# Kernel tuning notes

Hardware: AMD Instinct MI355X
Metric: run time of the kernel (lower is better)

Reference implementation:

```python
import jax, jax.numpy as jnp
import numpy as np

EMBED_DIM = 768
NUM_HEADS = 12
HEAD_DIM = EMBED_DIM // NUM_HEADS
SCALER = HEAD_DIM ** (-0.5)


def setup_inputs() -> dict:
    key = jax.random.key(0)
    k_x, k_wqkv, k_wo = jax.random.split(key, 3)
    B, N, C = 8, 1024, EMBED_DIM
    # GlorotUniform limits
    lim_qkv = (6.0 / (C + 3 * C)) ** 0.5
    lim_o = (6.0 / (C + C)) ** 0.5
    return {
        "inputs": jax.random.normal(k_x, (B, N, C), dtype=jnp.float32),
        "w_qkv": jax.random.uniform(k_wqkv, (C, 3 * C), minval=-lim_qkv, maxval=lim_qkv, dtype=jnp.float32),
        "b_qkv": jnp.zeros((3 * C,), dtype=jnp.float32),
        "w_out": jax.random.uniform(k_wo, (C, C), minval=-lim_o, maxval=lim_o, dtype=jnp.float32),
        "b_out": jnp.zeros((C,), dtype=jnp.float32),
    }


def reference(inputs, w_qkv, b_qkv, w_out, b_out):
    B, N, C = inputs.shape
    H, D = NUM_HEADS, C // NUM_HEADS
    qkv = inputs @ w_qkv + b_qkv                      # [B, N, 3C]
    qkv = qkv.reshape(B, N, 3, H, D).transpose(2, 0, 3, 1, 4)  # [3, B, H, N, D]
    q, k, v = qkv[0], qkv[1], qkv[2]
    scores = jnp.einsum("bhnd,bhmd->bhnm", q, k) * SCALER      # [B, H, N, N]
    attn = jax.nn.softmax(scores, axis=-1)
    x = jnp.einsum("bhnm,bhmd->bhnd", attn, v)                  # [B, H, N, D]
    x = x.transpose(0, 2, 1, 3).reshape(B, N, C)
    return x @ w_out + b_out
```

## Files before the change

kernel.cpp:

```cpp
#include <hip/hip_runtime.h>
#include <hip/hip_bf16.h>
#include <cstdint>
#include <cstddef>

#define EMBED 768
#define NHEADS 12
#define HDIM 64
#define SEQ 1024
#define BATCH 8

typedef __attribute__((ext_vector_type(8))) short bf16x8;
typedef __attribute__((ext_vector_type(4))) float f32x4;
typedef __attribute__((ext_vector_type(16))) float f32x16;
typedef __attribute__((ext_vector_type(4))) unsigned int u32x4;

__device__ __forceinline__ short f2bf(float f) {
    union { float f; uint32_t u; } x; x.f = f;
    uint32_t r = x.u + 0x7fffu + ((x.u >> 16) & 1u);
    return (short)(r >> 16);
}

__device__ __forceinline__ unsigned int cvt_pk_bf16(float lo, float hi) {
    unsigned int r;
    asm("v_cvt_pk_bf16_f32 %0, %1, %2" : "=v"(r) : "v"(lo), "v"(hi));
    return r;
}

__device__ __forceinline__ void permswap(unsigned int& a, unsigned int& b) {
    asm volatile("v_permlane32_swap_b32 %0, %1" : "+v"(a), "+v"(b));
}

__device__ __forceinline__ void gload_lds16(const void* g, void* l) {
    __builtin_amdgcn_global_load_lds(
        (const __attribute__((address_space(1))) unsigned int*)g,
        (__attribute__((address_space(3))) unsigned int*)l, 16, 0, 0);
}

__global__ __launch_bounds__(256) void convert_bf16(
    const float* __restrict__ in, short* __restrict__ out) {
    size_t i = ((size_t)blockIdx.x * 256 + threadIdx.x) * 8;
    float4 a = *reinterpret_cast<const float4*>(in + i);
    float4 b = *reinterpret_cast<const float4*>(in + i + 4);
    bf16x8 v;
    v[0] = f2bf(a.x); v[1] = f2bf(a.y); v[2] = f2bf(a.z); v[3] = f2bf(a.w);
    v[4] = f2bf(b.x); v[5] = f2bf(b.y); v[6] = f2bf(b.z); v[7] = f2bf(b.w);
    *reinterpret_cast<bf16x8*>(out + i) = v;
}

__global__ __launch_bounds__(256) void transpose_conv(
    const float* __restrict__ in, short* __restrict__ out, int R, int C) {
    __shared__ float tile[64][65];
    const int tid = threadIdx.x;
    const int c0 = blockIdx.x * 64, r0 = blockIdx.y * 64;
#pragma unroll
    for (int i = 0; i < 16; ++i) {
        int e = tid + 256 * i;
        int r = e >> 6, c = e & 63;
        tile[r][c] = in[(size_t)(r0 + r) * C + c0 + c];
    }
    __syncthreads();
#pragma unroll
    for (int i = 0; i < 16; ++i) {
        int e = tid + 256 * i;
        int rr = e >> 6, cc = e & 63;
        out[(size_t)(c0 + rr) * R + r0 + cc] = f2bf(tile[cc][rr]);
    }
}

__global__ __launch_bounds__(256) void gemm_qkv(
    const short* __restrict__ A, const short* __restrict__ Bt,
    const float* __restrict__ bias,
    short* __restrict__ Qo, short* __restrict__ Ko, short* __restrict__ Vto) {
    __shared__ __align__(16) char smem[65536];
    const int tid = threadIdx.x;
    const int lane = tid & 63;
    const int wid = tid >> 6;
    const int wm = wid >> 1, wn = wid & 1;
    const int bid = blockIdx.x;
    const int wg = (bid & 7) * 144 + (bid >> 3);
    const int mb = wg / 18, nb = wg - mb * 18;
    const int m0 = mb * 128;
    const int n0 = nb * 128;

    const f32x4 zero4 = {0.f, 0.f, 0.f, 0.f};
    f32x4 acc[4][4];
#pragma unroll
    for (int i = 0; i < 4; ++i)
#pragma unroll
        for (int j = 0; j < 4; ++j) acc[i][j] = zero4;

    const short* Ab = A + (size_t)m0 * EMBED;
    const short* Bb = Bt + (size_t)n0 * EMBED;

    auto stage = [&](int p, int kt) {
        const int k0 = kt * 64;
        char* base = smem + p * 32768;
#pragma unroll
        for (int i = 0; i < 4; ++i) {
            int e = i * 256 + tid;
            int r = e >> 3, cs = (e & 7) ^ (r & 7);
            char* dst = base + (size_t)(i * 256 + wid * 64) * 16;
            gload_lds16(Ab + (size_t)r * EMBED + k0 + cs * 8, dst);
            gload_lds16(Bb + (size_t)r * EMBED + k0 + cs * 8, dst + 16384);
        }
    };

    stage(0, 0);
    stage(1, 1);
    asm volatile("s_waitcnt vmcnt(8)" ::: "memory");
    __builtin_amdgcn_s_barrier();
    __builtin_amdgcn_sched_barrier(0);

    for (int t = 0; t < 12; ++t) {
        const int p = t & 1;
        const char* As = smem + p * 32768;
        const char* Bs = As + 16384;
        bf16x8 af[4][2], bfv[4][2];
#pragma unroll
        for (int mi = 0; mi < 4; ++mi)
#pragma unroll
            for (int kh = 0; kh < 2; ++kh) {
                int row = wm * 64 + mi * 16 + (lane & 15);
                int c = kh * 4 + (lane >> 4);
                af[mi][kh] = *reinterpret_cast<const bf16x8*>(
                    As + row * 128 + (((c ^ (row & 7))) << 4));
            }
#pragma unroll
        for (int ni = 0; ni < 4; ++ni)
#pragma unroll
            for (int kh = 0; kh < 2; ++kh) {
                int row = wn * 64 + ni * 16 + (lane & 15);
                int c = kh * 4 + (lane >> 4);
                bfv[ni][kh] = *reinterpret_cast<const bf16x8*>(
                    Bs + row * 128 + (((c ^ (row & 7))) << 4));
            }
        asm volatile("s_waitcnt lgkmcnt(0)" ::: "memory");
        __builtin_amdgcn_s_barrier();
        __builtin_amdgcn_sched_barrier(0);
        if (t + 2 < 12) stage(p, t + 2);

        __builtin_amdgcn_s_setprio(1);
#pragma unroll
        for (int mi = 0; mi < 4; ++mi)
#pragma unroll
            for (int ni = 0; ni < 4; ++ni)
#pragma unroll
                for (int kh = 0; kh < 2; ++kh)
                    acc[mi][ni] = __builtin_amdgcn_mfma_f32_16x16x32_bf16(
                        af[mi][kh], bfv[ni][kh], acc[mi][ni], 0, 0, 0);
        __builtin_amdgcn_s_setprio(0);

        if (t + 2 < 12)
            asm volatile("s_waitcnt vmcnt(8)" ::: "memory");
        else
            asm volatile("s_waitcnt vmcnt(0)" ::: "memory");
        __builtin_amdgcn_s_barrier();
        __builtin_amdgcn_sched_barrier(0);
    }

    const int s = nb / 6;
    const int bb = m0 >> 10;
    if (s == 2) {
        char* T = smem;
#pragma unroll
        for (int mi = 0; mi < 4; ++mi)
#pragma unroll
            for (int ni = 0; ni < 4; ++ni)
#pragma unroll
                for (int rp = 0; rp < 2; ++rp) {
                    int ml = wm * 64 + mi * 16 + ((lane >> 4) << 2) + rp * 2;
                    int nl = wn * 64 + ni * 16 + (lane & 15);
                    float bsv = bias[n0 + nl];
                    unsigned int w = cvt_pk_bf16(acc[mi][ni][rp * 2] + bsv,
                                                 acc[mi][ni][rp * 2 + 1] + bsv);
                    *reinterpret_cast<unsigned int*>(
                        T + nl * 256 + ((ml * 2) ^ ((nl & 7) << 4))) = w;
                }
        __syncthreads();
        short* Vrow0 = Vto + ((size_t)bb * 768 + (nb - 12) * 128) * SEQ + (m0 & 1023);
#pragma unroll
        for (int it = 0; it < 8; ++it) {
            int chunk = it * 256 + tid;
            int row = chunk >> 4, k = chunk & 15;
            u32x4 v = *reinterpret_cast<const u32x4*>(
                T + row * 256 + ((k * 16) ^ ((row & 7) << 4)));
            *reinterpret_cast<u32x4*>(Vrow0 + (size_t)row * SEQ + k * 8) = v;
        }
    } else {
        short* dst = (s == 0) ? Qo : Ko;
        const float qs = (s == 0) ? 0.18033688f : 1.0f;
        const int rem0 = n0 - s * 768;
#pragma unroll
        for (int mi = 0; mi < 4; ++mi)
#pragma unroll
            for (int ni = 0; ni < 4; ++ni)
#pragma unroll
                for (int r = 0; r < 4; ++r) {
                    int m = m0 + wm * 64 + mi * 16 + ((lane >> 4) << 2) + r;
                    int nl = wn * 64 + ni * 16 + (lane & 15);
                    int rem = rem0 + nl;
                    int h = rem >> 6, d = rem & 63;
                    int tok = m & 1023;
                    float v = (acc[mi][ni][r] + bias[n0 + nl]) * qs;
                    dst[(((size_t)(bb * NHEADS + h)) * SEQ + tok) * HDIM + d] = f2bf(v);
                }
    }
}

__global__ __launch_bounds__(256) void attn_kernel(
    const short* __restrict__ Q, const short* __restrict__ K,
    const short* __restrict__ Vt, short* __restrict__ Xo) {
    __shared__ __align__(16) char smem[49152];
    const int tid = threadIdx.x, lane = tid & 63, wid = tid >> 6;
    const int l31 = lane & 31, g = lane >> 5;
    const int bh = blockIdx.x, qt = blockIdx.y;
    const int b = bh / NHEADS, h = bh - b * NHEADS;
    const short* Qh = Q + (size_t)bh * SEQ * HDIM;
    const short* Kh = K + (size_t)bh * SEQ * HDIM;
    const short* Vh = Vt + (size_t)bh * HDIM * SEQ;
    const int q0 = qt * 128 + wid * 32;
    const int swz = (l31 & 7);

    const f32x16 zero16 = 0.f;
    bf16x8 qf[4];
#pragma unroll
    for (int ds = 0; ds < 4; ++ds)
        qf[ds] = *reinterpret_cast<const bf16x8*>(
            Qh + (size_t)(q0 + l31) * HDIM + ds * 16 + g * 8);

    u32x4 onesw;
    onesw[0] = 0x3f803f80u; onesw[1] = 0x3f803f80u;
    onesw[2] = 0x3f803f80u; onesw[3] = 0x3f803f80u;
    const bf16x8 ones = __builtin_bit_cast(bf16x8, onesw);

    f32x16 o0 = zero16, o1 = zero16;
    f32x16 ls = zero16;

    auto stage = [&](int buf, int j0) {
#pragma unroll
        for (int i = 0; i < 2; ++i) {
            int e = i * 256 + tid;
            int r = e >> 3, cs = (e & 7) ^ (r & 7);
            char* dst = smem + (size_t)(i * 256 + wid * 64) * 16 + buf * 8192;
            gload_lds16(Kh + (size_t)(j0 + r) * HDIM + cs * 8, dst);
            gload_lds16(Vh + (size_t)r * SEQ + j0 + cs * 8, dst + 24576);
        }
    };

    stage(0, 0);
    stage(1, 64);

    for (int t = 0; t < 16; ++t) {
        const int bsel = t % 3;
        if (t < 15)
            asm volatile("s_waitcnt vmcnt(4)" ::: "memory");
        else
            asm volatile("s_waitcnt vmcnt(0)" ::: "memory");
        __builtin_amdgcn_s_barrier();
        __builtin_amdgcn_sched_barrier(0);

        const char* kb = smem + bsel * 8192;
        const char* vb = smem + 24576 + bsel * 8192;

        bf16x8 kf[2][4];
#pragma unroll
        for (int s = 0; s < 2; ++s)
#pragma unroll
            for (int ds = 0; ds < 4; ++ds)
                kf[s][ds] = *reinterpret_cast<const bf16x8*>(
                    kb + (s * 32 + l31) * 128 + (((ds * 2 + g) ^ swz) << 4));
        bf16x8 vf[4][2];
#pragma unroll
        for (int kst = 0; kst < 4; ++kst)
#pragma unroll
            for (int dsub = 0; dsub < 2; ++dsub)
                vf[kst][dsub] = *reinterpret_cast<const bf16x8*>(
                    vb + (dsub * 32 + l31) * 128 + (((kst * 2 + g) ^ swz) << 4));
        __builtin_amdgcn_sched_barrier(0);
        if (t + 2 < 16) stage((t + 2) % 3, (t + 2) * 64);

        f32x16 s0 = zero16, s1 = zero16;
        __builtin_amdgcn_s_setprio(1);
#pragma unroll
        for (int ds = 0; ds < 4; ++ds) {
            s0 = __builtin_amdgcn_mfma_f32_32x32x16_bf16(kf[0][ds], qf[ds], s0, 0, 0, 0);
            s1 = __builtin_amdgcn_mfma_f32_32x32x16_bf16(kf[1][ds], qf[ds], s1, 0, 0, 0);
        }
        __builtin_amdgcn_s_setprio(0);

#pragma unroll
        for (int r = 0; r < 16; ++r) {
            s0[r] = __builtin_amdgcn_exp2f(s0[r]);
            s1[r] = __builtin_amdgcn_exp2f(s1[r]);
        }

        bf16x8 pf[4];
#pragma unroll
        for (int s = 0; s < 2; ++s) {
            const f32x16& sv = s ? s1 : s0;
            unsigned int pk[8];
#pragma unroll
            for (int j = 0; j < 8; ++j) pk[j] = cvt_pk_bf16(sv[2 * j], sv[2 * j + 1]);
            permswap(pk[0], pk[2]); permswap(pk[1], pk[3]);
            permswap(pk[4], pk[6]); permswap(pk[5], pk[7]);
            u32x4 wlo, whi;
            wlo[0] = pk[0]; wlo[1] = pk[1]; wlo[2] = pk[2]; wlo[3] = pk[3];
            whi[0] = pk[4]; whi[1] = pk[5]; whi[2] = pk[6]; whi[3] = pk[7];
            pf[s * 2 + 0] = __builtin_bit_cast(bf16x8, wlo);
            pf[s * 2 + 1] = __builtin_bit_cast(bf16x8, whi);
        }

        __builtin_amdgcn_s_setprio(1);
#pragma unroll
        for (int kst = 0; kst < 4; ++kst) {
            o0 = __builtin_amdgcn_mfma_f32_32x32x16_bf16(vf[kst][0], pf[kst], o0, 0, 0, 0);
            o1 = __builtin_amdgcn_mfma_f32_32x32x16_bf16(vf[kst][1], pf[kst], o1, 0, 0, 0);
            ls = __builtin_amdgcn_mfma_f32_32x32x16_bf16(ones, pf[kst], ls, 0, 0, 0);
        }
        __builtin_amdgcn_s_setprio(0);
    }

    const float rl = 1.0f / ls[0];

    __syncthreads();
    char* T = smem;
    {
        char* Tw = T + (wid * 32 + l31) * 128;
        const int qx = (l31 & 7) << 4;
#pragma unroll
        for (int half = 0; half < 2; ++half) {
            const f32x16& ov = half ? o1 : o0;
#pragma unroll
            for (int j = 0; j < 8; ++j) {
                unsigned int w = cvt_pk_bf16(ov[2 * j] * rl, ov[2 * j + 1] * rl);
                int off = 4 * (j & 1) + 16 * (j >> 1) + 8 * g + 64 * half;
                *reinterpret_cast<unsigned int*>(Tw + (off ^ qx)) = w;
            }
        }
    }
    __syncthreads();
    const int q0b = qt * 128;
    short* xbase = Xo + ((size_t)b * SEQ + q0b) * EMBED + h * HDIM;
#pragma unroll
    for (int it = 0; it < 4; ++it) {
        int chunk = it * 256 + tid;
        int row = chunk >> 3, k = chunk & 7;
        u32x4 v = *reinterpret_cast<const u32x4*>(
            T + row * 128 + ((k * 16) ^ ((row & 7) << 4)));
        *reinterpret_cast<u32x4*>(xbase + (size_t)row * EMBED + k * 8) = v;
    }
}

__global__ __launch_bounds__(256) void gemm_out(
    const short* __restrict__ A, const short* __restrict__ Bt,
    const float* __restrict__ bias, float* __restrict__ C) {
    __shared__ __align__(16) char smem[49152];
    const int tid = threadIdx.x;
    const int lane = tid & 63;
    const int wid = tid >> 6;
    const int wm = wid >> 1, wn = wid & 1;
    const int bid = blockIdx.x;
    const int wg = (bid & 7) * 96 + (bid >> 3);
    const int mb = wg / 12, nb = wg - mb * 12;
    const int m0 = mb * 128;
    const int n0 = nb * 64;

    const f32x4 zero4 = {0.f, 0.f, 0.f, 0.f};
    f32x4 acc[4][2];
#pragma unroll
    for (int i = 0; i < 4; ++i)
#pragma unroll
        for (int j = 0; j < 2; ++j) acc[i][j] = zero4;

    const short* Ab = A + (size_t)m0 * EMBED;
    const short* Bb = Bt + (size_t)n0 * EMBED;

    auto stage = [&](int p, int kt) {
        const int k0 = kt * 64;
        char* base = smem + p * 24576;
#pragma unroll
        for (int i = 0; i < 4; ++i) {
            int e = i * 256 + tid;
            int r = e >> 3, cs = (e & 7) ^ (r & 7);
            gload_lds16(Ab + (size_t)r * EMBED + k0 + cs * 8,
                        base + (size_t)(i * 256 + wid * 64) * 16);
        }
#pragma unroll
        for (int i = 0; i < 2; ++i) {
            int e = i * 256 + tid;
            int r = e >> 3, cs = (e & 7) ^ (r & 7);
            gload_lds16(Bb + (size_t)r * EMBED + k0 + cs * 8,
                        base + 16384 + (size_t)(i * 256 + wid * 64) * 16);
        }
    };

    stage(0, 0);
    stage(1, 1);
    asm volatile("s_waitcnt vmcnt(6)" ::: "memory");
    __builtin_amdgcn_s_barrier();
    __builtin_amdgcn_sched_barrier(0);

    for (int t = 0; t < 12; ++t) {
        const int p = t & 1;
        const char* As = smem + p * 24576;
        const char* Bs = As + 16384;
        bf16x8 af[4][2], bfv[2][2];
#pragma unroll
        for (int mi = 0; mi < 4; ++mi)
#pragma unroll
            for (int kh = 0; kh < 2; ++kh) {
                int row = wm * 64 + mi * 16 + (lane & 15);
                int c = kh * 4 + (lane >> 4);
                af[mi][kh] = *reinterpret_cast<const bf16x8*>(
                    As + row * 128 + (((c ^ (row & 7))) << 4));
            }
#pragma unroll
        for (int ni = 0; ni < 2; ++ni)
#pragma unroll
            for (int kh = 0; kh < 2; ++kh) {
                int row = wn * 32 + ni * 16 + (lane & 15);
                int c = kh * 4 + (lane >> 4);
                bfv[ni][kh] = *reinterpret_cast<const bf16x8*>(
                    Bs + row * 128 + (((c ^ (row & 7))) << 4));
            }
        asm volatile("s_waitcnt lgkmcnt(0)" ::: "memory");
        __builtin_amdgcn_s_barrier();
        __builtin_amdgcn_sched_barrier(0);
        if (t + 2 < 12) stage(p, t + 2);

        __builtin_amdgcn_s_setprio(1);
#pragma unroll
        for (int mi = 0; mi < 4; ++mi)
#pragma unroll
            for (int ni = 0; ni < 2; ++ni)
#pragma unroll
                for (int kh = 0; kh < 2; ++kh)
                    acc[mi][ni] = __builtin_amdgcn_mfma_f32_16x16x32_bf16(
                        af[mi][kh], bfv[ni][kh], acc[mi][ni], 0, 0, 0);
        __builtin_amdgcn_s_setprio(0);

        if (t + 2 < 12)
            asm volatile("s_waitcnt vmcnt(6)" ::: "memory");
        else
            asm volatile("s_waitcnt vmcnt(0)" ::: "memory");
        __builtin_amdgcn_s_barrier();
        __builtin_amdgcn_sched_barrier(0);
    }

#pragma unroll
    for (int mi = 0; mi < 4; ++mi)
#pragma unroll
        for (int ni = 0; ni < 2; ++ni)
#pragma unroll
            for (int r = 0; r < 4; ++r) {
                int m = m0 + wm * 64 + mi * 16 + ((lane >> 4) << 2) + r;
                int n = n0 + wn * 32 + ni * 16 + (lane & 15);
                C[(size_t)m * EMBED + n] = acc[mi][ni][r] + bias[n];
            }
}

extern "C" void kernel_launch(void* const* d_in, const int* in_sizes, int n_in,
                              void* d_out, int out_size, void* d_ws, size_t ws_size,
                              hipStream_t stream) {
    const float* x      = (const float*)d_in[0];
    const float* w_qkv  = (const float*)d_in[1];
    const float* b_qkv  = (const float*)d_in[2];
    const float* w_out  = (const float*)d_in[3];
    const float* b_out  = (const float*)d_in[4];
    float* out = (float*)d_out;
    char* ws = (char*)d_ws;

    short* wqkvT = (short*)(ws + 0);
    short* woutT = (short*)(ws + 3538944);
    short* Qb    = (short*)(ws + 4718592);
    short* Kb    = (short*)(ws + 17301504);
    short* Vtb   = (short*)(ws + 29884416);
    short* Xbf   = (short*)(ws + 42467328);
    short* Xab   = (short*)(ws + 42467328);

    convert_bf16<<<dim3(3072), 256, 0, stream>>>(x, Xbf);
    transpose_conv<<<dim3(36, 12), 256, 0, stream>>>(w_qkv, wqkvT, 768, 2304);
    transpose_conv<<<dim3(12, 12), 256, 0, stream>>>(w_out, woutT, 768, 768);
    gemm_qkv<<<dim3(1152), 256, 0, stream>>>(Xbf, wqkvT, b_qkv, Qb, Kb, Vtb);
    attn_kernel<<<dim3(96, 8), 256, 0, stream>>>(Qb, Kb, Vtb, Xab);
    gemm_out<<<dim3(768), 256, 0, stream>>>(Xab, woutT, b_out, out);
}
```

Before: 106.9 us.

## Process two query groups per wave in attention, halving waves per block

The attention kernel now runs 2 waves per block, and each wave handles 64 query rows as two 32-row groups. This lets each K/V fragment read from LDS be reused for twice as many MFMAs. The row-sum is now computed with VALU adds plus a cross-half shuffle, replacing the extra ones-vector MFMA, which removes a third of the PV-stage MFMAs. The cost is higher register pressure, fewer waves per block to hide latency, and more global-to-LDS loads issued per thread.

Measured after the change: 105.0 us. Within noise of the previous version (-1.8%).

```diff
diff --git a/kernel.cpp b/kernel.cpp
--- a/kernel.cpp
+++ b/kernel.cpp
@@ -207,7 +207,7 @@
     }
 }
 
-__global__ __launch_bounds__(256) void attn_kernel(
+__global__ __launch_bounds__(128, 2) void attn_kernel(
     const short* __restrict__ Q, const short* __restrict__ K,
     const short* __restrict__ Vt, short* __restrict__ Xo) {
     __shared__ __align__(16) char smem[49152];
@@ -218,30 +218,27 @@
     const short* Qh = Q + (size_t)bh * SEQ * HDIM;
     const short* Kh = K + (size_t)bh * SEQ * HDIM;
     const short* Vh = Vt + (size_t)bh * HDIM * SEQ;
-    const int q0 = qt * 128 + wid * 32;
+    const int q0 = qt * 128 + wid * 64;
     const int swz = (l31 & 7);
 
     const f32x16 zero16 = 0.f;
-    bf16x8 qf[4];
-#pragma unroll
-    for (int ds = 0; ds < 4; ++ds)
-        qf[ds] = *reinterpret_cast<const bf16x8*>(
-            Qh + (size_t)(q0 + l31) * HDIM + ds * 16 + g * 8);
-
-    u32x4 onesw;
-    onesw[0] = 0x3f803f80u; onesw[1] = 0x3f803f80u;
-    onesw[2] = 0x3f803f80u; onesw[3] = 0x3f803f80u;
-    const bf16x8 ones = __builtin_bit_cast(bf16x8, onesw);
-
-    f32x16 o0 = zero16, o1 = zero16;
-    f32x16 ls = zero16;
+    bf16x8 qf[2][4];
+#pragma unroll
+    for (int qg = 0; qg < 2; ++qg)
+#pragma unroll
+        for (int ds = 0; ds < 4; ++ds)
+            qf[qg][ds] = *reinterpret_cast<const bf16x8*>(
+                Qh + (size_t)(q0 + qg * 32 + l31) * HDIM + ds * 16 + g * 8);
+
+    f32x16 oA0 = zero16, oA1 = zero16, oB0 = zero16, oB1 = zero16;
+    float lA = 0.f, lB = 0.f;
 
     auto stage = [&](int buf, int j0) {
 #pragma unroll
-        for (int i = 0; i < 2; ++i) {
-            int e = i * 256 + tid;
+        for (int i = 0; i < 4; ++i) {
+            int e = i * 128 + tid;
             int r = e >> 3, cs = (e & 7) ^ (r & 7);
-            char* dst = smem + (size_t)(i * 256 + wid * 64) * 16 + buf * 8192;
+            char* dst = smem + (size_t)(i * 128 + wid * 64) * 16 + buf * 8192;
             gload_lds16(Kh + (size_t)(j0 + r) * HDIM + cs * 8, dst);
             gload_lds16(Vh + (size_t)r * SEQ + j0 + cs * 8, dst + 24576);
         }
@@ -253,7 +250,7 @@
     for (int t = 0; t < 16; ++t) {
         const int bsel = t % 3;
         if (t < 15)
-            asm volatile("s_waitcnt vmcnt(4)" ::: "memory");
+            asm volatile("s_waitcnt vmcnt(8)" ::: "memory");
         else
             asm volatile("s_waitcnt vmcnt(0)" ::: "memory");
         __builtin_amdgcn_s_barrier();
@@ -269,6 +266,50 @@
             for (int ds = 0; ds < 4; ++ds)
                 kf[s][ds] = *reinterpret_cast<const bf16x8*>(
                     kb + (s * 32 + l31) * 128 + (((ds * 2 + g) ^ swz) << 4));
+
+        f32x16 sA0 = zero16, sA1 = zero16, sB0 = zero16, sB1 = zero16;
+        __builtin_amdgcn_s_setprio(1);
+#pragma unroll
+        for (int ds = 0; ds < 4; ++ds) {
+            sA0 = __builtin_amdgcn_mfma_f32_32x32x16_bf16(kf[0][ds], qf[0][ds], sA0, 0, 0, 0);
+            sA1 = __builtin_amdgcn_mfma_f32_32x32x16_bf16(kf[1][ds], qf[0][ds], sA1, 0, 0, 0);
+            sB0 = __builtin_amdgcn_mfma_f32_32x32x16_bf16(kf[0][ds], qf[1][ds], sB0, 0, 0, 0);
+            sB1 = __builtin_amdgcn_mfma_f32_32x32x16_bf16(kf[1][ds], qf[1][ds], sB1, 0, 0, 0);
+        }
+        __builtin_amdgcn_s_setprio(0);
+
+        float rsA = 0.f, rsB = 0.f;
+#pragma unroll
+        for (int r = 0; r < 16; ++r) {
+            float a0 = __builtin_amdgcn_exp2f(sA0[r]);
+            float a1 = __builtin_amdgcn_exp2f(sA1[r]);
+            float b0 = __builtin_amdgcn_exp2f(sB0[r]);
+            float b1 = __builtin_amdgcn_exp2f(sB1[r]);
+            sA0[r] = a0; sA1[r] = a1; sB0[r] = b0; sB1[r] = b1;
+            rsA += a0 + a1; rsB += b0 + b1;
+        }
+        lA += rsA; lB += rsB;
+
+        bf16x8 pfA[4], pfB[4];
+#pragma unroll
+        for (int qg = 0; qg < 2; ++qg) {
+            bf16x8* pf = qg ? pfB : pfA;
+#pragma unroll
+            for (int s = 0; s < 2; ++s) {
+                const f32x16& sv = qg ? (s ? sB1 : sB0) : (s ? sA1 : sA0);
+                unsigned int pk[8];
+#pragma unroll
+                for (int j = 0; j < 8; ++j) pk[j] = cvt_pk_bf16(sv[2 * j], sv[2 * j + 1]);
+                permswap(pk[0], pk[2]); permswap(pk[1], pk[3]);
+                permswap(pk[4], pk[6]); permswap(pk[5], pk[7]);
+                u32x4 wlo, whi;
+                wlo[0] = pk[0]; wlo[1] = pk[1]; wlo[2] = pk[2]; wlo[3] = pk[3];
+                whi[0] = pk[4]; whi[1] = pk[5]; whi[2] = pk[6]; whi[3] = pk[7];
+                pf[s * 2 + 0] = __builtin_bit_cast(bf16x8, wlo);
+                pf[s * 2 + 1] = __builtin_bit_cast(bf16x8, whi);
+            }
+        }
+
         bf16x8 vf[4][2];
 #pragma unroll
         for (int kst = 0; kst < 4; ++kst)
@@ -279,62 +320,38 @@
         __builtin_amdgcn_sched_barrier(0);
         if (t + 2 < 16) stage((t + 2) % 3, (t + 2) * 64);
 
-        f32x16 s0 = zero16, s1 = zero16;
         __builtin_amdgcn_s_setprio(1);
 #pragma unroll
-        for (int ds = 0; ds < 4; ++ds) {
-            s0 = __builtin_amdgcn_mfma_f32_32x32x16_bf16(kf[0][ds], qf[ds], s0, 0, 0, 0);
-            s1 = __builtin_amdgcn_mfma_f32_32x32x16_bf16(kf[1][ds], qf[ds], s1, 0, 0, 0);
+        for (int kst = 0; kst < 4; ++kst) {
+            oA0 = __builtin_amdgcn_mfma_f32_32x32x16_bf16(vf[kst][0], pfA[kst], oA0, 0, 0, 0);
+            oA1 = __builtin_amdgcn_mfma_f32_32x32x16_bf16(vf[kst][1], pfA[kst], oA1, 0, 0, 0);
+            oB0 = __builtin_amdgcn_mfma_f32_32x32x16_bf16(vf[kst][0], pfB[kst], oB0, 0, 0, 0);
+            oB1 = __builtin_amdgcn_mfma_f32_32x32x16_bf16(vf[kst][1], pfB[kst], oB1, 0, 0, 0);
         }
         __builtin_amdgcn_s_setprio(0);
-
-#pragma unroll
-        for (int r = 0; r < 16; ++r) {
-            s0[r] = __builtin_amdgcn_exp2f(s0[r]);
-            s1[r] = __builtin_amdgcn_exp2f(s1[r]);
-        }
-
-        bf16x8 pf[4];
-#pragma unroll
-        for (int s = 0; s < 2; ++s) {
-            const f32x16& sv = s ? s1 : s0;
-            unsigned int pk[8];
-#pragma unroll
-            for (int j = 0; j < 8; ++j) pk[j] = cvt_pk_bf16(sv[2 * j], sv[2 * j + 1]);
-            permswap(pk[0], pk[2]); permswap(pk[1], pk[3]);
-            permswap(pk[4], pk[6]); permswap(pk[5], pk[7]);
-            u32x4 wlo, whi;
-            wlo[0] = pk[0]; wlo[1] = pk[1]; wlo[2] = pk[2]; wlo[3] = pk[3];
-            whi[0] = pk[4]; whi[1] = pk[5]; whi[2] = pk[6]; whi[3] = pk[7];
-            pf[s * 2 + 0] = __builtin_bit_cast(bf16x8, wlo);
-            pf[s * 2 + 1] = __builtin_bit_cast(bf16x8, whi);
-        }
-
-        __builtin_amdgcn_s_setprio(1);
-#pragma unroll
-        for (int kst = 0; kst < 4; ++kst) {
-            o0 = __builtin_amdgcn_mfma_f32_32x32x16_bf16(vf[kst][0], pf[kst], o0, 0, 0, 0);
-            o1 = __builtin_amdgcn_mfma_f32_32x32x16_bf16(vf[kst][1], pf[kst], o1, 0, 0, 0);
-            ls = __builtin_amdgcn_mfma_f32_32x32x16_bf16(ones, pf[kst], ls, 0, 0, 0);
-        }
-        __builtin_amdgcn_s_setprio(0);
-    }
-
-    const float rl = 1.0f / ls[0];
+    }
+
+    lA += __shfl_xor(lA, 32);
+    lB += __shfl_xor(lB, 32);
+    const float rlA = 1.0f / lA, rlB = 1.0f / lB;
 
     __syncthreads();
     char* T = smem;
     {
-        char* Tw = T + (wid * 32 + l31) * 128;
         const int qx = (l31 & 7) << 4;
 #pragma unroll
-        for (int half = 0; half < 2; ++half) {
-            const f32x16& ov = half ? o1 : o0;
-#pragma unroll
-            for (int j = 0; j < 8; ++j) {
-                unsigned int w = cvt_pk_bf16(ov[2 * j] * rl, ov[2 * j + 1] * rl);
-                int off = 4 * (j & 1) + 16 * (j >> 1) + 8 * g + 64 * half;
-                *reinterpret_cast<unsigned int*>(Tw + (off ^ qx)) = w;
+        for (int qg = 0; qg < 2; ++qg) {
+            char* Tw = T + (wid * 64 + qg * 32 + l31) * 128;
+            const float rl = qg ? rlB : rlA;
+#pragma unroll
+            for (int half = 0; half < 2; ++half) {
+                const f32x16& ov = qg ? (half ? oB1 : oB0) : (half ? oA1 : oA0);
+#pragma unroll
+                for (int j = 0; j < 8; ++j) {
+                    unsigned int w = cvt_pk_bf16(ov[2 * j] * rl, ov[2 * j + 1] * rl);
+                    int off = 4 * (j & 1) + 16 * (j >> 1) + 8 * g + 64 * half;
+                    *reinterpret_cast<unsigned int*>(Tw + (off ^ qx)) = w;
+                }
             }
         }
     }
@@ -342,8 +359,8 @@
     const int q0b = qt * 128;
     short* xbase = Xo + ((size_t)b * SEQ + q0b) * EMBED + h * HDIM;
 #pragma unroll
-    for (int it = 0; it < 4; ++it) {
-        int chunk = it * 256 + tid;
+    for (int it = 0; it < 8; ++it) {
+        int chunk = it * 128 + tid;
         int row = chunk >> 3, k = chunk & 7;
         u32x4 v = *reinterpret_cast<const u32x4*>(
             T + row * 128 + ((k * 16) ^ ((row & 7) << 4)));
@@ -482,6 +499,6 @@
     transpose_conv<<<dim3(36, 12), 256, 0, stream>>>(w_qkv, wqkvT, 768, 2304);
     transpose_conv<<<dim3(12, 12), 256, 0, stream>>>(w_out, woutT, 768, 768);
     gemm_qkv<<<dim3(1152), 256, 0, stream>>>(Xbf, wqkvT, b_qkv, Qb, Kb, Vtb);
-    attn_kernel<<<dim3(96, 8), 256, 0, stream>>>(Qb, Kb, Vtb, Xab);
+    attn_kernel<<<dim3(96, 8), 128, 0, stream>>>(Qb, Kb, Vtb, Xab);
     gemm_out<<<dim3(768), 256, 0, stream>>>(Xab, woutT, b_out, out);
 }
```
